# Performance work log

Hardware: AMD Instinct MI355X
Metric: run time of the kernel (lower is better)

## Reference

```python
import jax, jax.numpy as jnp
import numpy as np

N_NODES = 100000


def setup_inputs() -> dict:
    key = jax.random.key(0)
    k1, k2, k3, k4, k5, k6 = jax.random.split(key, 6)
    x = jax.random.normal(k1, (N_NODES, 256), dtype=jnp.float32)
    edge_index = jax.random.randint(k2, (2, 3200000), 0, N_NODES, dtype=jnp.int64)
    # GCNConv(256, 3): glorot weight + zero bias (PyG default)
    lim1 = float(np.sqrt(6.0 / (256 + 3)))
    W1 = jax.random.uniform(k3, (256, 3), minval=-lim1, maxval=lim1, dtype=jnp.float32)
    b1 = jnp.zeros((3,), dtype=jnp.float32)
    # Linear(3, 7): torch default kaiming-uniform-ish bounds
    lim2 = float(1.0 / np.sqrt(3))
    W2 = jax.random.uniform(k4, (3, 7), minval=-lim2, maxval=lim2, dtype=jnp.float32)
    b2 = jax.random.uniform(k5, (7,), minval=-lim2, maxval=lim2, dtype=jnp.float32)
    return {"x": x, "edge_index": edge_index, "W1": W1, "b1": b1, "W2": W2, "b2": b2}


def gcn_conv(x, edge_index, W, b, num_nodes):
    # PyG GCNConv: add self-loops, symmetric deg^-1/2 (A+I) deg^-1/2 normalization,
    # aggregate transformed features, then add bias.
    loop = jnp.arange(num_nodes, dtype=edge_index.dtype)
    src = jnp.concatenate([edge_index[0], loop])
    dst = jnp.concatenate([edge_index[1], loop])
    ones = jnp.ones_like(dst, dtype=x.dtype)
    deg = jax.ops.segment_sum(ones, dst, num_segments=num_nodes)  # [N]
    dinv = jnp.where(deg > 0, jax.lax.rsqrt(deg), 0.0)
    norm = dinv[src] * dinv[dst]  # [E+N]
    h = x @ W  # [N, 3] — transform BEFORE gather (small width)
    msg = h[src] * norm[:, None]  # [E+N, 3]
    agg = jax.ops.segment_sum(msg, dst, num_segments=num_nodes)  # [N, 3]
    return agg + b


def reference(x, edge_index, W1, b1, W2, b2):
    h = jax.nn.relu(gcn_conv(x, edge_index, W1, b1, x.shape[0]))  # [N, 3]
    z = h @ W2 + b2  # [N, 7]
    return (h, z)
```

## Files before the change

### kernel.cpp

```cpp
#include <hip/hip_runtime.h>
#include <stdint.h>


#define BSHIFT 8
#define BNODES 256
#define BPAD 392
#define CAPM 16384
#define SPLITC 8
#define NBX 1024

__device__ __forceinline__ bool ei_is64(const unsigned* __restrict__ ei) {
    const int t = threadIdx.x;
    const int nz = (t < 256) && (ei[2 * t + 1] != 0u);
    return __syncthreads_or(nz) == 0;
}

__global__ __launch_bounds__(512) void k_pre(const float* __restrict__ x,
                                             const float* __restrict__ W1,
                                             float4* __restrict__ part4,
                                             const unsigned* __restrict__ ei,
                                             unsigned* __restrict__ gtotal,
                                             unsigned* __restrict__ records,
                                             int E, int B, int CH, int nbin, int N) {
    const bool is64 = ei_is64(ei);
    if ((int)blockIdx.x < nbin) {
        __shared__ unsigned cnt[BPAD], base[BPAD], cur[BPAD];
        for (int i = threadIdx.x; i < BPAD; i += 512) { cnt[i] = 0u; cur[i] = 0u; }
        __syncthreads();
        const int e0 = blockIdx.x * CH;
        const int e1 = min(E, e0 + CH);
        if (is64) {
            const uint4* dp = (const uint4*)(ei + 2 * (size_t)E + 2 * e0);
            const int n2 = (e1 - e0) >> 1;
            for (int q = threadIdx.x; q < n2; q += 512) {
                const uint4 v = dp[q];
                atomicAdd(&cnt[v.x >> BSHIFT], 1u);
                atomicAdd(&cnt[v.z >> BSHIFT], 1u);
            }
            for (int e = e0 + 2 * n2 + threadIdx.x; e < e1; e += 512)
                atomicAdd(&cnt[ei[2 * (size_t)E + 2 * e] >> BSHIFT], 1u);
        } else {
            const uint4* dp = (const uint4*)(ei + (size_t)E + e0);
            const int n4 = (e1 - e0) >> 2;
            for (int q = threadIdx.x; q < n4; q += 512) {
                const uint4 v = dp[q];
                atomicAdd(&cnt[v.x >> BSHIFT], 1u);
                atomicAdd(&cnt[v.y >> BSHIFT], 1u);
                atomicAdd(&cnt[v.z >> BSHIFT], 1u);
                atomicAdd(&cnt[v.w >> BSHIFT], 1u);
            }
            for (int e = e0 + 4 * n4 + threadIdx.x; e < e1; e += 512)
                atomicAdd(&cnt[ei[(size_t)E + e] >> BSHIFT], 1u);
        }
        __syncthreads();
        for (int i = threadIdx.x; i < B; i += 512)
            base[i] = cnt[i] ? atomicAdd(&gtotal[i], cnt[i]) : 0u;
        __syncthreads();
        auto emit = [&](unsigned s, unsigned d) {
            const unsigned bb  = d >> BSHIFT;
            const unsigned idx = atomicAdd(&cur[bb], 1u);
            const unsigned pos = base[bb] + idx;
            if (pos < (unsigned)CAPM)
                records[(size_t)bb * CAPM + pos] = (s << BSHIFT) | (d & (BNODES - 1));
        };
        const int nq = (e1 - e0) >> 2;
        if (is64) {
            const unsigned long long* e64 = (const unsigned long long*)ei;
            const ulonglong2* sp = (const ulonglong2*)(e64 + e0);
            const ulonglong2* dp = (const ulonglong2*)(e64 + (size_t)E + e0);
            for (int q = threadIdx.x; q < nq; q += 512) {
                const ulonglong2 sa = sp[2 * q], sb = sp[2 * q + 1];
                const ulonglong2 da = dp[2 * q], db = dp[2 * q + 1];
                emit((unsigned)sa.x, (unsigned)da.x);
                emit((unsigned)sa.y, (unsigned)da.y);
                emit((unsigned)sb.x, (unsigned)db.x);
                emit((unsigned)sb.y, (unsigned)db.y);
            }
            for (int e = e0 + 4 * nq + threadIdx.x; e < e1; e += 512)
                emit((unsigned)e64[e], (unsigned)e64[(size_t)E + e]);
        } else {
            const uint4* sp = (const uint4*)(ei + e0);
            const uint4* dp = (const uint4*)(ei + (size_t)E + e0);
            for (int q = threadIdx.x; q < nq; q += 512) {
                const uint4 s4 = sp[q], d4 = dp[q];
                emit(s4.x, d4.x);
                emit(s4.y, d4.y);
                emit(s4.z, d4.z);
                emit(s4.w, d4.w);
            }
            for (int e = e0 + 4 * nq + threadIdx.x; e < e1; e += 512)
                emit(ei[e], ei[(size_t)E + e]);
        }
    } else {
        const int bx     = blockIdx.x - nbin;
        const int gtid   = bx * 512 + threadIdx.x;
        const int nwaves = (((int)gridDim.x - nbin) * 512) >> 6;
        const int wave   = gtid >> 6;
        const int lane   = threadIdx.x & 63;
        const int fg     = lane & 15;
        const int m      = lane >> 4;
        const int f      = wave & 3;
        const int wq     = wave >> 2;
        const int wstep  = nwaves >> 2;
        float w[4][3];
#pragma unroll
        for (int j = 0; j < 4; ++j)
#pragma unroll
            for (int c = 0; c < 3; ++c)
                w[j][c] = W1[(f * 64 + fg * 4 + j) * 3 + c];
        const int nq = (N + 3) >> 2;
        for (int q = wq; q < nq; q += 4 * wstep) {
            int nd[4]; bool ok[4]; float4 v[4];
#pragma unroll
            for (int u = 0; u < 4; ++u) {
                const int qu = q + u * wstep;
                nd[u] = qu * 4 + m;
                ok[u] = (qu < nq) && (nd[u] < N);
                v[u]  = ok[u] ? *reinterpret_cast<const float4*>(
                                    x + (size_t)nd[u] * 256 + f * 64 + fg * 4)
                              : make_float4(0.f, 0.f, 0.f, 0.f);
            }
#pragma unroll
            for (int u = 0; u < 4; ++u) {
                float s0 = v[u].x * w[0][0] + v[u].y * w[1][0] + v[u].z * w[2][0] + v[u].w * w[3][0];
                float s1 = v[u].x * w[0][1] + v[u].y * w[1][1] + v[u].z * w[2][1] + v[u].w * w[3][1];
                float s2 = v[u].x * w[0][2] + v[u].y * w[1][2] + v[u].z * w[2][2] + v[u].w * w[3][2];
#pragma unroll
                for (int off = 8; off >= 1; off >>= 1) {
                    s0 += __shfl_xor(s0, off, 64);
                    s1 += __shfl_xor(s1, off, 64);
                    s2 += __shfl_xor(s2, off, 64);
                }
                if (ok[u] && fg == 0)
                    part4[(size_t)f * N + nd[u]] = make_float4(s0, s1, s2, 0.f);
            }
        }
    }
}

__global__ __launch_bounds__(256) void k_cnt2(const unsigned* __restrict__ records,
                                              const unsigned* __restrict__ total,
                                              unsigned* __restrict__ pcount) {
    __shared__ unsigned cnt[BNODES];
    const int b  = blockIdx.x >> 3;
    const int sl = blockIdx.x & 7;
    cnt[threadIdx.x] = 0u;
    __syncthreads();
    int n = (int)total[b]; if (n > CAPM) n = CAPM;
    const int chunk = (n + SPLITC - 1) / SPLITC;
    const int lo = sl * chunk;
    const int hi = min(n, lo + chunk);
    const unsigned* rec = records + (size_t)b * CAPM;
    int i = lo + threadIdx.x;
    for (; i + 256 < hi; i += 512) {
        const unsigned r0 = rec[i], r1 = rec[i + 256];
        atomicAdd(&cnt[r0 & (BNODES - 1)], 1u);
        atomicAdd(&cnt[r1 & (BNODES - 1)], 1u);
    }
    if (i < hi) atomicAdd(&cnt[rec[i] & (BNODES - 1)], 1u);
    __syncthreads();
    pcount[((size_t)blockIdx.x << BSHIFT) + threadIdx.x] = cnt[threadIdx.x];
}

__global__ __launch_bounds__(256) void k_dinv2(const float4* __restrict__ part4,
                                               const unsigned* __restrict__ pcount,
                                               float* __restrict__ g4, int N) {
    const int i = blockIdx.x * 256 + threadIdx.x;
    if (i >= N) return;
    const int b = i >> BSHIFT, t = i & (BNODES - 1);
    const float4 p0 = part4[i];
    const float4 p1 = part4[(size_t)N + i];
    const float4 p2 = part4[(size_t)2 * N + i];
    const float4 p3 = part4[(size_t)3 * N + i];
    const float hx = p0.x + p1.x + p2.x + p3.x;
    const float hy = p0.y + p1.y + p2.y + p3.y;
    const float hz = p0.z + p1.z + p2.z + p3.z;
    unsigned deg = 1u;
#pragma unroll
    for (int s = 0; s < SPLITC; ++s)
        deg += pcount[(((size_t)b * SPLITC + s) << BSHIFT) + t];
    const float r = rsqrtf((float)deg);
    reinterpret_cast<float4*>(g4)[i] = make_float4(hx * r, hy * r, hz * r, r);
}

__global__ __launch_bounds__(256) void k_msg2(const unsigned* __restrict__ records,
                                              const unsigned* __restrict__ total,
                                              const float* __restrict__ g4,
                                              float* __restrict__ psum) {
    __shared__ float acc[BNODES * 3];
    const int b  = blockIdx.x >> 3;
    const int sl = blockIdx.x & 7;
    for (int i = threadIdx.x; i < BNODES * 3; i += 256) acc[i] = 0.f;
    __syncthreads();
    int n = (int)total[b]; if (n > CAPM) n = CAPM;
    const int chunk = (n + SPLITC - 1) / SPLITC;
    const int lo = sl * chunk;
    const int hi = min(n, lo + chunk);
    const unsigned* rec = records + (size_t)b * CAPM;
    const float4* g4v = reinterpret_cast<const float4*>(g4);
    int i = lo + threadIdx.x;
    for (; i + 256 < hi; i += 512) {
        const unsigned r0 = rec[i], r1 = rec[i + 256];
        const float4 ga = g4v[r0 >> BSHIFT];
        const float4 gb = g4v[r1 >> BSHIFT];
        const unsigned l0 = (r0 & (BNODES - 1)) * 3, l1 = (r1 & (BNODES - 1)) * 3;
        atomicAdd(&acc[l0 + 0], ga.x); atomicAdd(&acc[l0 + 1], ga.y); atomicAdd(&acc[l0 + 2], ga.z);
        atomicAdd(&acc[l1 + 0], gb.x); atomicAdd(&acc[l1 + 1], gb.y); atomicAdd(&acc[l1 + 2], gb.z);
    }
    if (i < hi) {
        const unsigned r0 = rec[i];
        const float4 ga = g4v[r0 >> BSHIFT];
        const unsigned l0 = (r0 & (BNODES - 1)) * 3;
        atomicAdd(&acc[l0 + 0], ga.x); atomicAdd(&acc[l0 + 1], ga.y); atomicAdd(&acc[l0 + 2], ga.z);
    }
    __syncthreads();
    const size_t base = ((size_t)blockIdx.x * 3) << BSHIFT;
    psum[base +   0 + threadIdx.x] = acc[threadIdx.x * 3 + 0];
    psum[base + 256 + threadIdx.x] = acc[threadIdx.x * 3 + 1];
    psum[base + 512 + threadIdx.x] = acc[threadIdx.x * 3 + 2];
}

__global__ __launch_bounds__(256) void k_fin(const float* __restrict__ psum,
                                             const float* __restrict__ g4,
                                             const float* __restrict__ b1,
                                             const float* __restrict__ W2,
                                             const float* __restrict__ b2,
                                             float* __restrict__ out, int N) {
    const int i = blockIdx.x * 256 + threadIdx.x;
    if (i >= N) return;
    const int b = i >> BSHIFT, t = i & (BNODES - 1);
    float a0 = 0.f, a1 = 0.f, a2 = 0.f;
#pragma unroll
    for (int s = 0; s < SPLITC; ++s) {
        const size_t base = (((size_t)b * SPLITC + s) * 3) << BSHIFT;
        a0 += psum[base + t];
        a1 += psum[base + 256 + t];
        a2 += psum[base + 512 + t];
    }
    const float4 g = reinterpret_cast<const float4*>(g4)[i];
    const float  r = g.w;
    const float h0 = fmaxf(r * (a0 + g.x) + b1[0], 0.f);
    const float h1 = fmaxf(r * (a1 + g.y) + b1[1], 0.f);
    const float h2 = fmaxf(r * (a2 + g.z) + b1[2], 0.f);
    out[3 * (size_t)i + 0] = h0;
    out[3 * (size_t)i + 1] = h1;
    out[3 * (size_t)i + 2] = h2;
    float* z = out + (size_t)3 * N;
#pragma unroll
    for (int c = 0; c < 7; ++c)
        z[7 * (size_t)i + c] = h0 * W2[c] + h1 * W2[7 + c] + h2 * W2[14 + c] + b2[c];
}

__global__ __launch_bounds__(256) void k_xw1_fb(const float* __restrict__ x,
                                                const float* __restrict__ W1,
                                                float* __restrict__ g4,
                                                unsigned* __restrict__ zptr,
                                                int nzero, int N) {
    const int gtid = blockIdx.x * 256 + threadIdx.x;
    const int nthread = gridDim.x * 256;
    for (int i = gtid; i < nzero; i += nthread) zptr[i] = 0u;
    const int lane = threadIdx.x & 63;
    float w[4][3];
#pragma unroll
    for (int k = 0; k < 4; ++k)
#pragma unroll
        for (int c = 0; c < 3; ++c) w[k][c] = W1[(lane * 4 + k) * 3 + c];
    const int wave = gtid >> 6, nwaves = nthread >> 6;
    for (int node = wave; node < N; node += nwaves) {
        const float4 v = *reinterpret_cast<const float4*>(x + (size_t)node * 256 + lane * 4);
        float s0 = v.x * w[0][0] + v.y * w[1][0] + v.z * w[2][0] + v.w * w[3][0];
        float s1 = v.x * w[0][1] + v.y * w[1][1] + v.z * w[2][1] + v.w * w[3][1];
        float s2 = v.x * w[0][2] + v.y * w[1][2] + v.z * w[2][2] + v.w * w[3][2];
#pragma unroll
        for (int off = 32; off > 0; off >>= 1) {
            s0 += __shfl_xor(s0, off, 64);
            s1 += __shfl_xor(s1, off, 64);
            s2 += __shfl_xor(s2, off, 64);
        }
        if (lane == 0)
            reinterpret_cast<float4*>(g4)[node] = make_float4(s0, s1, s2, 0.f);
    }
}
__global__ __launch_bounds__(256) void k_deg_fb(const unsigned* __restrict__ ei,
                                                float* __restrict__ deg, int E) {
    const bool is64 = ei_is64(ei);
    const int e = blockIdx.x * 256 + threadIdx.x;
    if (e >= E) return;
    const unsigned d = is64 ? (unsigned)((const unsigned long long*)ei)[(size_t)E + e]
                            : ei[(size_t)E + e];
    atomicAdd(&deg[d], 1.0f);
}
__global__ __launch_bounds__(256) void k_dinv_fb(const float* __restrict__ deg,
                                                 float* __restrict__ g4, int N) {
    const int i = blockIdx.x * 256 + threadIdx.x;
    if (i >= N) return;
    const float r = rsqrtf(1.0f + deg[i]);
    const float4 h = reinterpret_cast<const float4*>(g4)[i];
    reinterpret_cast<float4*>(g4)[i] = make_float4(h.x * r, h.y * r, h.z * r, r);
}
__global__ __launch_bounds__(256) void k_edge_fb(const unsigned* __restrict__ ei,
                                                 const float* __restrict__ g4,
                                                 float* __restrict__ u4, int E) {
    const bool is64 = ei_is64(ei);
    const int e = blockIdx.x * 256 + threadIdx.x;
    if (e >= E) return;
    unsigned s, d;
    if (is64) {
        const unsigned long long* q = (const unsigned long long*)ei;
        s = (unsigned)q[e]; d = (unsigned)q[(size_t)E + e];
    } else {
        s = ei[e]; d = ei[(size_t)E + e];
    }
    const float4 g = reinterpret_cast<const float4*>(g4)[s];
    atomicAdd(&u4[4 * (size_t)d + 0], g.x);
    atomicAdd(&u4[4 * (size_t)d + 1], g.y);
    atomicAdd(&u4[4 * (size_t)d + 2], g.z);
}
__global__ __launch_bounds__(256) void k_final_fb(const float* __restrict__ u4,
                                                  const float* __restrict__ g4,
                                                  const float* __restrict__ b1,
                                                  const float* __restrict__ W2,
                                                  const float* __restrict__ b2,
                                                  float* __restrict__ out, int N) {
    const int i = blockIdx.x * 256 + threadIdx.x;
    if (i >= N) return;
    const float4 g = reinterpret_cast<const float4*>(g4)[i];
    const float4 u = reinterpret_cast<const float4*>(u4)[i];
    const float  r = g.w;
    const float h0 = fmaxf(r * (u.x + g.x) + b1[0], 0.f);
    const float h1 = fmaxf(r * (u.y + g.y) + b1[1], 0.f);
    const float h2 = fmaxf(r * (u.z + g.z) + b1[2], 0.f);
    out[3 * (size_t)i + 0] = h0;
    out[3 * (size_t)i + 1] = h1;
    out[3 * (size_t)i + 2] = h2;
    float* z = out + (size_t)3 * N;
#pragma unroll
    for (int c = 0; c < 7; ++c)
        z[7 * (size_t)i + c] = h0 * W2[c] + h1 * W2[7 + c] + h2 * W2[14 + c] + b2[c];
}

extern "C" void kernel_launch(void* const* d_in, const int* in_sizes, int n_in,
                              void* d_out, int out_size, void* d_ws, size_t ws_size,
                              hipStream_t stream) {
    const float*    x   = (const float*)d_in[0];
    const unsigned* ei  = (const unsigned*)d_in[1];
    const float*    W1  = (const float*)d_in[2];
    const float*    b1  = (const float*)d_in[3];
    const float*    W2  = (const float*)d_in[4];
    const float*    b2  = (const float*)d_in[5];
    float*          out = (float*)d_out;

    const int N = in_sizes[0] / 256;
    const int E = in_sizes[1] / 2;
    const int B = (N + BNODES - 1) >> BSHIFT;

    const int CH   = ((E + 255) / 256 + 3) & ~3;
    const int nbin = (E + CH - 1) / CH;

    char* ws = (char*)d_ws;
    size_t off = 256;
    float*    g4      = (float*)(ws + off);
    off = (off + 16ull * N + 255) & ~(size_t)255;
    float4*   part4   = (float4*)(ws + off);
    off = (off + 64ull * N + 255) & ~(size_t)255;
    unsigned* gtotal  = (unsigned*)(ws + off);
    off = (off + 4ull * B + 255) & ~(size_t)255;
    unsigned* pcount  = (unsigned*)(ws + off);
    float*    psum    = (float*)(ws + off);
    off = (off + 4ull * B * SPLITC * 768 + 255) & ~(size_t)255;
    unsigned* records = (unsigned*)(ws + off);
    const size_t need = off + 4ull * B * CAPM + 4096;

    if (ws_size >= need) {
        hipMemsetAsync(gtotal, 0, 4ull * B, stream);
        k_pre<<<nbin + NBX, 512, 0, stream>>>(x, W1, part4, ei, gtotal, records,
                                              E, B, CH, nbin, N);
        k_cnt2<<<B * SPLITC, 256, 0, stream>>>(records, gtotal, pcount);
        k_dinv2<<<(N + 255) / 256, 256, 0, stream>>>(part4, pcount, g4, N);
        k_msg2<<<B * SPLITC, 256, 0, stream>>>(records, gtotal, g4, psum);
        k_fin<<<(N + 255) / 256, 256, 0, stream>>>(psum, g4, b1, W2, b2, out, N);
    } else {
        float* deg = (float*)part4;
        float* u4  = deg + N;
        k_xw1_fb<<<4096, 256, 0, stream>>>(x, W1, g4, (unsigned*)deg, 5 * N, N);
        k_deg_fb<<<(E + 255) / 256, 256, 0, stream>>>(ei, deg, E);
        k_dinv_fb<<<(N + 255) / 256, 256, 0, stream>>>(deg, g4, N);
        k_edge_fb<<<(E + 255) / 256, 256, 0, stream>>>(ei, g4, u4, E);
        k_final_fb<<<(N + 255) / 256, 256, 0, stream>>>(u4, g4, b1, W2, b2, out, N);
    }
}
```

Baseline: 118.8 us.

## Fuse degree count with dinv kernel, unroll record loops by four, enlarge binning chunks

Merges the split degree-count kernel and the dinv/normalize kernel into one kernel per 256-node bucket, which drops the pcount partial-count buffer and one launch. Each block now counts the whole bucket's records itself instead of using eight slices. The message-accumulation loop is unrolled to four independent record loads and gathers in flight, to hide gather latency. The edge-binning chunk size in the pre-kernel is tripled, which cuts the number of binning blocks. In exchange the degree kernel has less parallelism (B blocks instead of 8B).

```diff
diff --git a/kernel.cpp b/kernel.cpp
--- a/kernel.cpp
+++ b/kernel.cpp
@@ -138,49 +138,40 @@
     }
 }
 
-__global__ __launch_bounds__(256) void k_cnt2(const unsigned* __restrict__ records,
-                                              const unsigned* __restrict__ total,
-                                              unsigned* __restrict__ pcount) {
+__global__ __launch_bounds__(256) void k_deg(const unsigned* __restrict__ records,
+                                             const unsigned* __restrict__ gtotal,
+                                             const float4* __restrict__ part4,
+                                             float* __restrict__ g4, int N) {
     __shared__ unsigned cnt[BNODES];
-    const int b  = blockIdx.x >> 3;
-    const int sl = blockIdx.x & 7;
+    const int b = blockIdx.x;
     cnt[threadIdx.x] = 0u;
     __syncthreads();
-    int n = (int)total[b]; if (n > CAPM) n = CAPM;
-    const int chunk = (n + SPLITC - 1) / SPLITC;
-    const int lo = sl * chunk;
-    const int hi = min(n, lo + chunk);
+    int n = (int)gtotal[b]; if (n > CAPM) n = CAPM;
     const unsigned* rec = records + (size_t)b * CAPM;
-    int i = lo + threadIdx.x;
-    for (; i + 256 < hi; i += 512) {
-        const unsigned r0 = rec[i], r1 = rec[i + 256];
+    for (int i = threadIdx.x; i < n; i += 1024) {
+        const bool v1 = (i + 256) < n, v2 = (i + 512) < n, v3 = (i + 768) < n;
+        const unsigned r0 = rec[i];
+        const unsigned r1 = v1 ? rec[i + 256] : 0u;
+        const unsigned r2 = v2 ? rec[i + 512] : 0u;
+        const unsigned r3 = v3 ? rec[i + 768] : 0u;
         atomicAdd(&cnt[r0 & (BNODES - 1)], 1u);
-        atomicAdd(&cnt[r1 & (BNODES - 1)], 1u);
-    }
-    if (i < hi) atomicAdd(&cnt[rec[i] & (BNODES - 1)], 1u);
+        if (v1) atomicAdd(&cnt[r1 & (BNODES - 1)], 1u);
+        if (v2) atomicAdd(&cnt[r2 & (BNODES - 1)], 1u);
+        if (v3) atomicAdd(&cnt[r3 & (BNODES - 1)], 1u);
+    }
     __syncthreads();
-    pcount[((size_t)blockIdx.x << BSHIFT) + threadIdx.x] = cnt[threadIdx.x];
-}
-
-__global__ __launch_bounds__(256) void k_dinv2(const float4* __restrict__ part4,
-                                               const unsigned* __restrict__ pcount,
-                                               float* __restrict__ g4, int N) {
-    const int i = blockIdx.x * 256 + threadIdx.x;
-    if (i >= N) return;
-    const int b = i >> BSHIFT, t = i & (BNODES - 1);
-    const float4 p0 = part4[i];
-    const float4 p1 = part4[(size_t)N + i];
-    const float4 p2 = part4[(size_t)2 * N + i];
-    const float4 p3 = part4[(size_t)3 * N + i];
-    const float hx = p0.x + p1.x + p2.x + p3.x;
-    const float hy = p0.y + p1.y + p2.y + p3.y;
-    const float hz = p0.z + p1.z + p2.z + p3.z;
-    unsigned deg = 1u;
-#pragma unroll
-    for (int s = 0; s < SPLITC; ++s)
-        deg += pcount[(((size_t)b * SPLITC + s) << BSHIFT) + t];
-    const float r = rsqrtf((float)deg);
-    reinterpret_cast<float4*>(g4)[i] = make_float4(hx * r, hy * r, hz * r, r);
+    const int node = (b << BSHIFT) + threadIdx.x;
+    if (node < N) {
+        const float4 p0 = part4[node];
+        const float4 p1 = part4[(size_t)N + node];
+        const float4 p2 = part4[(size_t)2 * N + node];
+        const float4 p3 = part4[(size_t)3 * N + node];
+        const float hx = p0.x + p1.x + p2.x + p3.x;
+        const float hy = p0.y + p1.y + p2.y + p3.y;
+        const float hz = p0.z + p1.z + p2.z + p3.z;
+        const float r = rsqrtf(1.0f + (float)cnt[threadIdx.x]);
+        reinterpret_cast<float4*>(g4)[node] = make_float4(hx * r, hy * r, hz * r, r);
+    }
 }
 
 __global__ __launch_bounds__(256) void k_msg2(const unsigned* __restrict__ records,
@@ -198,20 +189,30 @@
     const int hi = min(n, lo + chunk);
     const unsigned* rec = records + (size_t)b * CAPM;
     const float4* g4v = reinterpret_cast<const float4*>(g4);
-    int i = lo + threadIdx.x;
-    for (; i + 256 < hi; i += 512) {
-        const unsigned r0 = rec[i], r1 = rec[i + 256];
-        const float4 ga = g4v[r0 >> BSHIFT];
-        const float4 gb = g4v[r1 >> BSHIFT];
-        const unsigned l0 = (r0 & (BNODES - 1)) * 3, l1 = (r1 & (BNODES - 1)) * 3;
-        atomicAdd(&acc[l0 + 0], ga.x); atomicAdd(&acc[l0 + 1], ga.y); atomicAdd(&acc[l0 + 2], ga.z);
-        atomicAdd(&acc[l1 + 0], gb.x); atomicAdd(&acc[l1 + 1], gb.y); atomicAdd(&acc[l1 + 2], gb.z);
-    }
-    if (i < hi) {
+    for (int i = lo + threadIdx.x; i < hi; i += 1024) {
+        const bool v1 = (i + 256) < hi, v2 = (i + 512) < hi, v3 = (i + 768) < hi;
         const unsigned r0 = rec[i];
-        const float4 ga = g4v[r0 >> BSHIFT];
+        const unsigned r1 = v1 ? rec[i + 256] : 0u;
+        const unsigned r2 = v2 ? rec[i + 512] : 0u;
+        const unsigned r3 = v3 ? rec[i + 768] : 0u;
+        const float4 g0 = g4v[r0 >> BSHIFT];
+        const float4 g1 = g4v[r1 >> BSHIFT];
+        const float4 g2 = g4v[r2 >> BSHIFT];
+        const float4 g3 = g4v[r3 >> BSHIFT];
         const unsigned l0 = (r0 & (BNODES - 1)) * 3;
-        atomicAdd(&acc[l0 + 0], ga.x); atomicAdd(&acc[l0 + 1], ga.y); atomicAdd(&acc[l0 + 2], ga.z);
+        atomicAdd(&acc[l0 + 0], g0.x); atomicAdd(&acc[l0 + 1], g0.y); atomicAdd(&acc[l0 + 2], g0.z);
+        if (v1) {
+            const unsigned l1 = (r1 & (BNODES - 1)) * 3;
+            atomicAdd(&acc[l1 + 0], g1.x); atomicAdd(&acc[l1 + 1], g1.y); atomicAdd(&acc[l1 + 2], g1.z);
+        }
+        if (v2) {
+            const unsigned l2 = (r2 & (BNODES - 1)) * 3;
+            atomicAdd(&acc[l2 + 0], g2.x); atomicAdd(&acc[l2 + 1], g2.y); atomicAdd(&acc[l2 + 2], g2.z);
+        }
+        if (v3) {
+            const unsigned l3 = (r3 & (BNODES - 1)) * 3;
+            atomicAdd(&acc[l3 + 0], g3.x); atomicAdd(&acc[l3 + 1], g3.y); atomicAdd(&acc[l3 + 2], g3.z);
+        }
     }
     __syncthreads();
     const size_t base = ((size_t)blockIdx.x * 3) << BSHIFT;
@@ -354,7 +355,7 @@
     const int E = in_sizes[1] / 2;
     const int B = (N + BNODES - 1) >> BSHIFT;
 
-    const int CH   = ((E + 255) / 256 + 3) & ~3;
+    const int CH   = ((E + 767) / 768 + 3) & ~3;
     const int nbin = (E + CH - 1) / CH;
 
     char* ws = (char*)d_ws;
@@ -365,7 +366,6 @@
     off = (off + 64ull * N + 255) & ~(size_t)255;
     unsigned* gtotal  = (unsigned*)(ws + off);
     off = (off + 4ull * B + 255) & ~(size_t)255;
-    unsigned* pcount  = (unsigned*)(ws + off);
     float*    psum    = (float*)(ws + off);
     off = (off + 4ull * B * SPLITC * 768 + 255) & ~(size_t)255;
     unsigned* records = (unsigned*)(ws + off);
@@ -375,8 +375,7 @@
         hipMemsetAsync(gtotal, 0, 4ull * B, stream);
         k_pre<<<nbin + NBX, 512, 0, stream>>>(x, W1, part4, ei, gtotal, records,
                                               E, B, CH, nbin, N);
-        k_cnt2<<<B * SPLITC, 256, 0, stream>>>(records, gtotal, pcount);
-        k_dinv2<<<(N + 255) / 256, 256, 0, stream>>>(part4, pcount, g4, N);
+        k_deg<<<B, 256, 0, stream>>>(records, gtotal, part4, g4, N);
         k_msg2<<<B * SPLITC, 256, 0, stream>>>(records, gtotal, g4, psum);
         k_fin<<<(N + 255) / 256, 256, 0, stream>>>(psum, g4, b1, W2, b2, out, N);
     } else {
```

Result: slower. 136.4 us (+14.9%).
